# Kernel tuning notes

Hardware: AMD Instinct MI355X
Metric: run time of the kernel (lower is better)

## Reference

```python
import jax, jax.numpy as jnp
import numpy as np

N_NODES = 100000
N_EDGES = 1600000
IN_DIM = 128
HID = 128
N_CLS = 10
N_GRAPHS = 128


def setup_inputs() -> dict:
    key = jax.random.key(0)
    ks = jax.random.split(key, 8)
    x = jax.random.normal(ks[0], (N_NODES, IN_DIM), dtype=jnp.float32)
    edge_index = jax.random.randint(ks[1], (2, N_EDGES), 0, N_NODES, dtype=jnp.int64)
    batch = jnp.sort(jax.random.randint(ks[2], (N_NODES,), 0, N_GRAPHS, dtype=jnp.int64))
    # GCNConv weights (PyG uses glorot; scale approximated) and biases
    W1 = jax.random.normal(ks[3], (IN_DIM, HID), dtype=jnp.float32) * (1.0 / np.sqrt(IN_DIM))
    b1 = jnp.zeros((HID,), dtype=jnp.float32)
    W2 = jax.random.normal(ks[4], (HID, HID), dtype=jnp.float32) * (1.0 / np.sqrt(HID))
    b2 = jnp.zeros((HID,), dtype=jnp.float32)
    Wlin = jax.random.normal(ks[5], (HID, N_CLS), dtype=jnp.float32) * (1.0 / np.sqrt(HID))
    blin = jnp.zeros((N_CLS,), dtype=jnp.float32)
    return {"x": x, "edge_index": edge_index, "batch": batch,
            "W1": W1, "b1": b1, "W2": W2, "b2": b2, "Wlin": Wlin, "blin": blin}


def _gcn_norm(edge_index, n_nodes):
    # PyG GCNConv default: add self-loops, symmetric D^-1/2 A D^-1/2 normalization
    loop = jnp.arange(n_nodes, dtype=edge_index.dtype)
    row = jnp.concatenate([edge_index[0], loop])  # source nodes
    col = jnp.concatenate([edge_index[1], loop])  # destination nodes
    ones = jnp.ones(col.shape[0], dtype=jnp.float32)
    deg = jax.ops.segment_sum(ones, col, num_segments=n_nodes)
    dinv = jnp.where(deg > 0, jax.lax.rsqrt(deg), 0.0)
    norm = dinv[row] * dinv[col]  # per-edge normalization coefficient
    return row, col, norm


def _gcn_conv(x, W, b, row, col, norm, n_nodes):
    h = x @ W                                   # [N, hid] dense transform first (small hid)
    msg = h[row] * norm[:, None]                # gather + scale over edges
    out = jax.ops.segment_sum(msg, col, num_segments=n_nodes)  # scatter-add aggregation
    return out + b


def reference(x, edge_index, batch, W1, b1, W2, b2, Wlin, blin):
    n = x.shape[0]
    row, col, norm = _gcn_norm(edge_index, n)
    h = jax.nn.relu(_gcn_conv(x, W1, b1, row, col, norm, n))
    h = jax.nn.relu(_gcn_conv(h, W2, b2, row, col, norm, n))
    # global_mean_pool over batch ids
    sums = jax.ops.segment_sum(h, batch, num_segments=N_GRAPHS)
    cnts = jax.ops.segment_sum(jnp.ones((n,), dtype=h.dtype), batch, num_segments=N_GRAPHS)
    pooled = sums / jnp.maximum(cnts, 1.0)[:, None]
    return pooled @ Wlin + blin  # [N_GRAPHS, n_cls]
```

## Files before the change

### kernel.cpp

```cpp
#include <hip/hip_runtime.h>

#define NN 100000
#define NE 1600000
#define DD 128
#define NG 128
#define NC 10
#define AGG_WAVES 8192
#define POOL_WAVES 2048

#define B1SH 8
#define NB1 ((NN + 255) / 256)
#define EPB 8192
#define NWG1 ((NE + EPB - 1) / EPB)
#define GEMM_BLOCKS ((NN + 63) / 64)

typedef __attribute__((ext_vector_type(8))) short short8v;
typedef __attribute__((ext_vector_type(4))) float f32x4;

__device__ __forceinline__ unsigned short f2bf(float f) {
    unsigned int u = __float_as_uint(f);
    u = (u + 0x7fffu + ((u >> 16) & 1u)) >> 16;
    return (unsigned short)u;
}
__device__ __forceinline__ float bflo(unsigned int p) { return __uint_as_float(p << 16); }
__device__ __forceinline__ float bfhi(unsigned int p) { return __uint_as_float(p & 0xffff0000u); }

__global__ __launch_bounds__(256) void hist_k(const int* __restrict__ col, int* __restrict__ hist) {
    __shared__ int lh[NB1];
    int t = threadIdx.x, w = blockIdx.x;
    for (int i = t; i < NB1; i += 256) lh[i] = 0;
    __syncthreads();
    int base = w * EPB;
    int lim = min(base + EPB, NE);
#pragma unroll 4
    for (int e = base + t; e < lim; e += 256) atomicAdd(&lh[col[e] >> B1SH], 1);
    __syncthreads();
    for (int i = t; i < NB1; i += 256) hist[i * NWG1 + w] = lh[i];
}

__global__ __launch_bounds__(512) void btot_k(const int* __restrict__ hist, int* __restrict__ bbase) {
    __shared__ int tmp[512];
    int t = threadIdx.x;
    int s = 0;
    if (t < NB1) {
        const int* hp = hist + t * NWG1;
        for (int w = 0; w < NWG1; ++w) s += hp[w];
    }
    tmp[t] = s;
    __syncthreads();
    for (int o = 1; o < 512; o <<= 1) {
        int v = (t >= o) ? tmp[t - o] : 0;
        __syncthreads();
        tmp[t] += v;
        __syncthreads();
    }
    if (t < NB1) bbase[t] = tmp[t] - s;
    if (t == 511) bbase[NB1] = tmp[511];
}

__global__ __launch_bounds__(256) void histscan_k(const int* __restrict__ bbase, int* __restrict__ hist) {
    __shared__ int tmp[256];
    int b = blockIdx.x, t = threadIdx.x;
    int v = (t < NWG1) ? hist[b * NWG1 + t] : 0;
    tmp[t] = v;
    __syncthreads();
    for (int o = 1; o < 256; o <<= 1) {
        int u = (t >= o) ? tmp[t - o] : 0;
        __syncthreads();
        tmp[t] += u;
        __syncthreads();
    }
    int excl = tmp[t] - v;
    if (t < NWG1) hist[b * NWG1 + t] = bbase[b] + excl;
}

__global__ __launch_bounds__(256) void part1_k(const int* __restrict__ row, const int* __restrict__ col,
                                               const int* __restrict__ hist, int* __restrict__ tmpe) {
    __shared__ int lcur[NB1];
    int t = threadIdx.x, w = blockIdx.x;
    for (int i = t; i < NB1; i += 256) lcur[i] = hist[i * NWG1 + w];
    __syncthreads();
    int base = w * EPB;
    int lim = min(base + EPB, NE);
#pragma unroll 4
    for (int e = base + t; e < lim; e += 256) {
        int c = col[e];
        int pos = atomicAdd(&lcur[c >> B1SH], 1);
        tmpe[pos] = (row[e] << B1SH) | (c & 255);
    }
}

__global__ __launch_bounds__(512) void part2b_k(const int* __restrict__ bbase, const int* __restrict__ tmpe,
                                                unsigned int* __restrict__ csr_src, int* __restrict__ offs,
                                                float* __restrict__ dinv) {
    __shared__ int lcnt[256];
    __shared__ int lsc[256];
    int b = blockIdx.x, t = threadIdx.x;
    if (t < 256) lcnt[t] = 0;
    __syncthreads();
    int ebeg = bbase[b], eend = bbase[b + 1];
    for (int e = ebeg + t; e < eend; e += 512) atomicAdd(&lcnt[tmpe[e] & 255], 1);
    __syncthreads();
    if (t < 256) lsc[t] = lcnt[t];
    __syncthreads();
    for (int o = 1; o < 256; o <<= 1) {
        int v = (t < 256 && t >= o) ? lsc[t - o] : 0;
        __syncthreads();
        if (t < 256) lsc[t] += v;
        __syncthreads();
    }
    int n0 = b << B1SH;
    if (t < 256) {
        int node = n0 + t;
        if (node < NN) {
            int excl = lsc[t] - lcnt[t];
            offs[node] = ebeg + excl;
            dinv[node] = rsqrtf((float)lcnt[t] + 1.0f);
        }
    }
    if (b == NB1 - 1 && t == 0) offs[NN] = NE;
    __syncthreads();
    if (t < 256) lsc[t] = ebeg + (lsc[t] - lcnt[t]);
    __syncthreads();
    for (int e = ebeg + t; e < eend; e += 512) {
        int p = tmpe[e];
        int pos = atomicAdd(&lsc[p & 255], 1);
        csr_src[pos] = (unsigned int)(p >> B1SH) << 6;
    }
}

__global__ __launch_bounds__(256) void pack_w2_k(const float* __restrict__ W1, const float* __restrict__ W2,
                                                 unsigned short* __restrict__ Wpk1,
                                                 unsigned short* __restrict__ Wpk2,
                                                 float* __restrict__ gsum) {
    int t = threadIdx.x;
    if (blockIdx.x == 2) {
        float4* g4 = (float4*)gsum;
        for (int i = t; i < NG * DD / 4; i += 256) g4[i] = make_float4(0, 0, 0, 0);
        return;
    }
    const float* W = blockIdx.x ? W2 : W1;
    unsigned short* Wpk = blockIdx.x ? Wpk2 : Wpk1;
    for (int f = t * 64; f < t * 64 + 64; ++f) {
        int j = f & 7, lane = (f >> 3) & 63, kk = (f >> 9) & 3, n = f >> 11;
        int k = kk * 32 + ((lane >> 4) << 3) + j;
        int c = n * 16 + (lane & 15);
        Wpk[f] = f2bf(W[k * DD + c]);
    }
}

template <int IN_BF16>
__global__ __launch_bounds__(256) void gemm_mfma_k(const void* __restrict__ Xv,
                                                   const unsigned short* __restrict__ Wpk,
                                                   const float* __restrict__ dinv,
                                                   unsigned short* __restrict__ outb) {
    __shared__ unsigned short wlds[16384];
    int tid = threadIdx.x;
    const uint4* wg = (const uint4*)Wpk;
    uint4* wl = (uint4*)wlds;
#pragma unroll
    for (int i = 0; i < 8; ++i) wl[tid + i * 256] = wg[tid + i * 256];
    __syncthreads();

    int w = tid >> 6, lane = tid & 63;
    int kg = lane >> 4;
    int rowbase = blockIdx.x * 64 + w * 16;
    int rl = min(rowbase + (lane & 15), NN - 1);

    short8v a[4];
    if (IN_BF16) {
        const unsigned short* xb = (const unsigned short*)Xv;
#pragma unroll
        for (int kk = 0; kk < 4; ++kk)
            a[kk] = *(const short8v*)(xb + (long)rl * DD + kk * 32 + kg * 8);
    } else {
        const float* xf = (const float*)Xv;
#pragma unroll
        for (int kk = 0; kk < 4; ++kk) {
            float4 f0 = *(const float4*)(xf + (long)rl * DD + kk * 32 + kg * 8);
            float4 f1 = *(const float4*)(xf + (long)rl * DD + kk * 32 + kg * 8 + 4);
            short8v t;
            t[0] = (short)f2bf(f0.x); t[1] = (short)f2bf(f0.y);
            t[2] = (short)f2bf(f0.z); t[3] = (short)f2bf(f0.w);
            t[4] = (short)f2bf(f1.x); t[5] = (short)f2bf(f1.y);
            t[6] = (short)f2bf(f1.z); t[7] = (short)f2bf(f1.w);
            a[kk] = t;
        }
    }

    f32x4 acc[8];
#pragma unroll
    for (int n = 0; n < 8; ++n) acc[n] = (f32x4){0.f, 0.f, 0.f, 0.f};
#pragma unroll
    for (int n = 0; n < 8; ++n) {
#pragma unroll
        for (int kk = 0; kk < 4; ++kk) {
            short8v b = *(const short8v*)(wlds + ((n * 4 + kk) * 64 + lane) * 8);
            acc[n] = __builtin_amdgcn_mfma_f32_16x16x32_bf16(a[kk], b, acc[n], 0, 0, 0);
        }
    }

    int c0 = lane & 15;
#pragma unroll
    for (int reg = 0; reg < 4; ++reg) {
        int row = rowbase + kg * 4 + reg;
        if (row < NN) {
            float dv = dinv[row];
            unsigned short* op = outb + (long)row * DD + c0;
#pragma unroll
            for (int n = 0; n < 8; ++n) op[n * 16] = f2bf(dv * acc[n][reg]);
        }
    }
}

__global__ __launch_bounds__(256) void agg_k(const unsigned int* __restrict__ hpb,
                                             const float* __restrict__ dinv,
                                             const int* __restrict__ offs,
                                             const unsigned int* __restrict__ csr,
                                             const float* __restrict__ bias,
                                             unsigned short* __restrict__ outb) {
    int wv = (blockIdx.x << 2) + (threadIdx.x >> 6);
    unsigned int lane = threadIdx.x & 63;
    float2 bb = ((const float2*)bias)[lane];
    for (int node = wv; node < NN; node += AGG_WAVES) {
        int s = offs[node];
        int e_end = offs[node + 1];
        unsigned int ps = hpb[(unsigned int)node * 64u + lane];
        float accx = bflo(ps);
        float accy = bfhi(ps);
        int e = s;
        for (; e + 8 <= e_end; e += 8) {
            unsigned int p0 = hpb[csr[e] + lane];
            unsigned int p1 = hpb[csr[e + 1] + lane];
            unsigned int p2 = hpb[csr[e + 2] + lane];
            unsigned int p3 = hpb[csr[e + 3] + lane];
            unsigned int p4 = hpb[csr[e + 4] + lane];
            unsigned int p5 = hpb[csr[e + 5] + lane];
            unsigned int p6 = hpb[csr[e + 6] + lane];
            unsigned int p7 = hpb[csr[e + 7] + lane];
            accx += (bflo(p0) + bflo(p1)) + (bflo(p2) + bflo(p3)) +
                    (bflo(p4) + bflo(p5)) + (bflo(p6) + bflo(p7));
            accy += (bfhi(p0) + bfhi(p1)) + (bfhi(p2) + bfhi(p3)) +
                    (bfhi(p4) + bfhi(p5)) + (bfhi(p6) + bfhi(p7));
        }
        if (e + 4 <= e_end) {
            unsigned int p0 = hpb[csr[e] + lane];
            unsigned int p1 = hpb[csr[e + 1] + lane];
            unsigned int p2 = hpb[csr[e + 2] + lane];
            unsigned int p3 = hpb[csr[e + 3] + lane];
            accx += (bflo(p0) + bflo(p1)) + (bflo(p2) + bflo(p3));
            accy += (bfhi(p0) + bfhi(p1)) + (bfhi(p2) + bfhi(p3));
            e += 4;
        }
        for (; e < e_end; ++e) {
            unsigned int p0 = hpb[csr[e] + lane];
            accx += bflo(p0);
            accy += bfhi(p0);
        }
        float dv = dinv[node];
        float ox = fmaxf(fmaf(dv, accx, bb.x), 0.0f);
        float oy = fmaxf(fmaf(dv, accy, bb.y), 0.0f);
        ((ushort2*)outb)[(unsigned int)node * 64u + lane] = make_ushort2(f2bf(ox), f2bf(oy));
    }
}

__global__ __launch_bounds__(256) void pool2_k(const unsigned short* __restrict__ h,
                                               const int* __restrict__ batch,
                                               float* __restrict__ gsum) {
    int wave = (blockIdx.x * 256 + threadIdx.x) >> 6;
    int lane = threadIdx.x & 63;
    const int per = (NN + POOL_WAVES - 1) / POOL_WAVES;
    int s = wave * per;
    int e = min(s + per, NN);
    if (s >= e) return;
    const unsigned int* h2 = (const unsigned int*)h;
    float2 acc = {0.0f, 0.0f};
    int cur = batch[s];
    for (int r = s; r < e; ++r) {
        int b = batch[r];
        if (b != cur) {
            atomicAdd(&gsum[cur * DD + 2 * lane], acc.x);
            atomicAdd(&gsum[cur * DD + 2 * lane + 1], acc.y);
            acc.x = 0.0f; acc.y = 0.0f;
            cur = b;
        }
        unsigned int v = h2[(unsigned int)r * 64u + lane];
        acc.x += bflo(v);
        acc.y += bfhi(v);
    }
    atomicAdd(&gsum[cur * DD + 2 * lane], acc.x);
    atomicAdd(&gsum[cur * DD + 2 * lane + 1], acc.y);
}

__global__ __launch_bounds__(256) void final_k(const float* __restrict__ gsum, const int* __restrict__ batch,
                                               const float* __restrict__ Wlin, const float* __restrict__ blin,
                                               float* __restrict__ out) {
    int idx = blockIdx.x * 256 + threadIdx.x;
    if (idx >= NG * NC) return;
    int g = idx / NC, c = idx % NC;
    int s0, s1;
    {
        int lo = 0, hi = NN;
        while (lo < hi) { int m = (lo + hi) >> 1; if (batch[m] < g) lo = m + 1; else hi = m; }
        s0 = lo;
        lo = s0; hi = NN;
        while (lo < hi) { int m = (lo + hi) >> 1; if (batch[m] < g + 1) lo = m + 1; else hi = m; }
        s1 = lo;
    }
    int cnt = s1 - s0;
    float inv = 1.0f / fmaxf((float)cnt, 1.0f);
    float acc = blin[c];
    for (int k = 0; k < DD; ++k) acc = fmaf(gsum[g * DD + k] * inv, Wlin[k * NC + c], acc);
    out[idx] = acc;
}

extern "C" void kernel_launch(void* const* d_in, const int* in_sizes, int n_in,
                              void* d_out, int out_size, void* d_ws, size_t ws_size,
                              hipStream_t stream) {
    const float* x     = (const float*)d_in[0];
    const int*   ei    = (const int*)d_in[1];
    const int*   batch = (const int*)d_in[2];
    const float* W1    = (const float*)d_in[3];
    const float* b1    = (const float*)d_in[4];
    const float* W2    = (const float*)d_in[5];
    const float* b2    = (const float*)d_in[6];
    const float* Wlin  = (const float*)d_in[7];
    const float* blin  = (const float*)d_in[8];
    float* out = (float*)d_out;

    const int* erow = ei;
    const int* ecol = ei + NE;

    char* ws = (char*)d_ws;
    size_t off = 0;
    auto alloc = [&](size_t bytes) {
        void* p = ws + off;
        off = (off + bytes + 255) & ~(size_t)255;
        return p;
    };
    unsigned short* hbuf  = (unsigned short*)alloc((size_t)NN * DD * 2);
    unsigned short* habuf = (unsigned short*)alloc((size_t)NN * DD * 2);
    unsigned short* Wpk1  = (unsigned short*)alloc(16384 * 2);
    unsigned short* Wpk2  = (unsigned short*)alloc(16384 * 2);
    float* dinv     = (float*)alloc(NN * 4);
    int*   offs     = (int*)alloc((NN + 1) * 4);
    int*   bbase    = (int*)alloc((NB1 + 1) * 4);
    int*   hist     = (int*)alloc((size_t)NB1 * NWG1 * 4);
    int*   tmpe     = (int*)alloc((size_t)NE * 4);
    unsigned int* csrsrc = (unsigned int*)alloc((size_t)NE * 4);
    float* gsum     = (float*)alloc(NG * DD * 4);
    (void)ws_size; (void)in_sizes; (void)n_in; (void)out_size;

    pack_w2_k<<<3, 256, 0, stream>>>(W1, W2, Wpk1, Wpk2, gsum);
    hist_k<<<NWG1, 256, 0, stream>>>(ecol, hist);
    btot_k<<<1, 512, 0, stream>>>(hist, bbase);
    histscan_k<<<NB1, 256, 0, stream>>>(bbase, hist);
    part1_k<<<NWG1, 256, 0, stream>>>(erow, ecol, hist, tmpe);
    part2b_k<<<NB1, 512, 0, stream>>>(bbase, tmpe, csrsrc, offs, dinv);

    gemm_mfma_k<0><<<GEMM_BLOCKS, 256, 0, stream>>>(x, Wpk1, dinv, hbuf);
    agg_k<<<AGG_WAVES / 4, 256, 0, stream>>>((const unsigned int*)hbuf, dinv, offs, csrsrc, b1, habuf);
    gemm_mfma_k<1><<<GEMM_BLOCKS, 256, 0, stream>>>(habuf, Wpk2, dinv, hbuf);
    agg_k<<<AGG_WAVES / 4, 256, 0, stream>>>((const unsigned int*)hbuf, dinv, offs, csrsrc, b2, habuf);

    pool2_k<<<POOL_WAVES / 4, 256, 0, stream>>>(habuf, batch, gsum);
    final_k<<<(NG * NC + 255) / 256, 256, 0, stream>>>(gsum, batch, Wlin, blin, out);
}
```

Before: 265.7 us.

## Fuse first GEMM with edge histogram and second aggregation with mean pooling

The first layer's x@W1 GEMM now runs in the same launch as the edge histogram, as separate blocks, so it no longer waits for the CSR build. Because dinv is not ready at that point, a new scale kernel applies the dinv row scaling afterwards. The second aggregation now accumulates pooled sums directly instead of writing the full hidden tensor and reading it back in a separate pool kernel. Trade-offs: an extra read-modify-write pass over hbuf for scaling, a bf16 rounding of the unscaled GEMM output before scaling, and contiguous node ranges per wave in the fused aggregation, which may balance load worse than the strided assignment.

```diff
diff --git a/kernel.cpp b/kernel.cpp
--- a/kernel.cpp
+++ b/kernel.cpp
@@ -6,7 +6,6 @@
 #define NG 128
 #define NC 10
 #define AGG_WAVES 8192
-#define POOL_WAVES 2048
 
 #define B1SH 8
 #define NB1 ((NN + 255) / 256)
@@ -25,17 +24,145 @@
 __device__ __forceinline__ float bflo(unsigned int p) { return __uint_as_float(p << 16); }
 __device__ __forceinline__ float bfhi(unsigned int p) { return __uint_as_float(p & 0xffff0000u); }
 
-__global__ __launch_bounds__(256) void hist_k(const int* __restrict__ col, int* __restrict__ hist) {
-    __shared__ int lh[NB1];
-    int t = threadIdx.x, w = blockIdx.x;
-    for (int i = t; i < NB1; i += 256) lh[i] = 0;
-    __syncthreads();
-    int base = w * EPB;
-    int lim = min(base + EPB, NE);
+template <int IN_BF16>
+__device__ __forceinline__ void gemm_body(const void* __restrict__ Xv,
+                                          const unsigned short* __restrict__ Wpk,
+                                          const float* __restrict__ dinv,
+                                          unsigned short* __restrict__ outb, int blk,
+                                          unsigned short* wlds) {
+    int tid = threadIdx.x;
+    const uint4* wg = (const uint4*)Wpk;
+    uint4* wl = (uint4*)wlds;
+#pragma unroll
+    for (int i = 0; i < 8; ++i) wl[tid + i * 256] = wg[tid + i * 256];
+    __syncthreads();
+
+    int w = tid >> 6, lane = tid & 63;
+    int kg = lane >> 4;
+    int rowbase = blk * 64 + w * 16;
+    int rl = min(rowbase + (lane & 15), NN - 1);
+
+    short8v a[4];
+    if (IN_BF16) {
+        const unsigned short* xb = (const unsigned short*)Xv;
+#pragma unroll
+        for (int kk = 0; kk < 4; ++kk)
+            a[kk] = *(const short8v*)(xb + (long)rl * DD + kk * 32 + kg * 8);
+    } else {
+        const float* xf = (const float*)Xv;
+#pragma unroll
+        for (int kk = 0; kk < 4; ++kk) {
+            float4 f0 = *(const float4*)(xf + (long)rl * DD + kk * 32 + kg * 8);
+            float4 f1 = *(const float4*)(xf + (long)rl * DD + kk * 32 + kg * 8 + 4);
+            short8v t;
+            t[0] = (short)f2bf(f0.x); t[1] = (short)f2bf(f0.y);
+            t[2] = (short)f2bf(f0.z); t[3] = (short)f2bf(f0.w);
+            t[4] = (short)f2bf(f1.x); t[5] = (short)f2bf(f1.y);
+            t[6] = (short)f2bf(f1.z); t[7] = (short)f2bf(f1.w);
+            a[kk] = t;
+        }
+    }
+
+    f32x4 acc[8];
+#pragma unroll
+    for (int n = 0; n < 8; ++n) acc[n] = (f32x4){0.f, 0.f, 0.f, 0.f};
+#pragma unroll
+    for (int n = 0; n < 8; ++n) {
+#pragma unroll
+        for (int kk = 0; kk < 4; ++kk) {
+            short8v b = *(const short8v*)(wlds + ((n * 4 + kk) * 64 + lane) * 8);
+            acc[n] = __builtin_amdgcn_mfma_f32_16x16x32_bf16(a[kk], b, acc[n], 0, 0, 0);
+        }
+    }
+
+    int c0 = lane & 15;
+#pragma unroll
+    for (int reg = 0; reg < 4; ++reg) {
+        int row = rowbase + kg * 4 + reg;
+        if (row < NN) {
+            float dv = dinv[row];
+            unsigned short* op = outb + (long)row * DD + c0;
+#pragma unroll
+            for (int n = 0; n < 8; ++n) op[n * 16] = f2bf(dv * acc[n][reg]);
+        }
+    }
+}
+
+__global__ __launch_bounds__(256) void k1_fused(const int* __restrict__ col, int* __restrict__ hist,
+                                                const float* __restrict__ x,
+                                                const unsigned short* __restrict__ Wpk1,
+                                                unsigned short* __restrict__ hbuf) {
+    __shared__ unsigned short wlds[16384];
+    int bid = blockIdx.x, t = threadIdx.x;
+    if (bid < NWG1) {
+        int* lh = (int*)wlds;
+        for (int i = t; i < NB1; i += 256) lh[i] = 0;
+        __syncthreads();
+        int base = bid * EPB;
+        int lim = min(base + EPB, NE);
 #pragma unroll 4
-    for (int e = base + t; e < lim; e += 256) atomicAdd(&lh[col[e] >> B1SH], 1);
-    __syncthreads();
-    for (int i = t; i < NB1; i += 256) hist[i * NWG1 + w] = lh[i];
+        for (int e = base + t; e < lim; e += 256) atomicAdd(&lh[col[e] >> B1SH], 1);
+        __syncthreads();
+        for (int i = t; i < NB1; i += 256) hist[i * NWG1 + bid] = lh[i];
+    } else {
+        int tid = threadIdx.x;
+        const uint4* wg = (const uint4*)Wpk1;
+        uint4* wl = (uint4*)wlds;
+#pragma unroll
+        for (int i = 0; i < 8; ++i) wl[tid + i * 256] = wg[tid + i * 256];
+        __syncthreads();
+        int w = tid >> 6, lane = tid & 63;
+        int kg = lane >> 4;
+        int blk = bid - NWG1;
+        int rowbase = blk * 64 + w * 16;
+        int rl = min(rowbase + (lane & 15), NN - 1);
+        short8v a[4];
+        const float* xf = x;
+#pragma unroll
+        for (int kk = 0; kk < 4; ++kk) {
+            float4 f0 = *(const float4*)(xf + (long)rl * DD + kk * 32 + kg * 8);
+            float4 f1 = *(const float4*)(xf + (long)rl * DD + kk * 32 + kg * 8 + 4);
+            short8v tv;
+            tv[0] = (short)f2bf(f0.x); tv[1] = (short)f2bf(f0.y);
+            tv[2] = (short)f2bf(f0.z); tv[3] = (short)f2bf(f0.w);
+            tv[4] = (short)f2bf(f1.x); tv[5] = (short)f2bf(f1.y);
+            tv[6] = (short)f2bf(f1.z); tv[7] = (short)f2bf(f1.w);
+            a[kk] = tv;
+        }
+        f32x4 acc[8];
+#pragma unroll
+        for (int n = 0; n < 8; ++n) acc[n] = (f32x4){0.f, 0.f, 0.f, 0.f};
+#pragma unroll
+        for (int n = 0; n < 8; ++n) {
+#pragma unroll
+            for (int kk = 0; kk < 4; ++kk) {
+                short8v b = *(const short8v*)(wlds + ((n * 4 + kk) * 64 + lane) * 8);
+                acc[n] = __builtin_amdgcn_mfma_f32_16x16x32_bf16(a[kk], b, acc[n], 0, 0, 0);
+            }
+        }
+        int c0 = lane & 15;
+#pragma unroll
+        for (int reg = 0; reg < 4; ++reg) {
+            int row = rowbase + kg * 4 + reg;
+            if (row < NN) {
+                unsigned short* op = hbuf + (long)row * DD + c0;
+#pragma unroll
+                for (int n = 0; n < 8; ++n) op[n * 16] = f2bf(acc[n][reg]);
+            }
+        }
+    }
+}
+
+__global__ __launch_bounds__(256) void scale1_k(unsigned int* __restrict__ hpb,
+                                                const float* __restrict__ dinv) {
+    int wv = (blockIdx.x << 2) + (threadIdx.x >> 6);
+    unsigned int lane = threadIdx.x & 63;
+    for (int row = wv; row < NN; row += AGG_WAVES) {
+        float dv = dinv[row];
+        unsigned int p = hpb[(unsigned int)row * 64u + lane];
+        hpb[(unsigned int)row * 64u + lane] =
+            ((unsigned int)f2bf(dv * bflo(p))) | ((unsigned int)f2bf(dv * bfhi(p)) << 16);
+    }
 }
 
 __global__ __launch_bounds__(512) void btot_k(const int* __restrict__ hist, int* __restrict__ bbase) {
@@ -149,67 +276,46 @@
     }
 }
 
-template <int IN_BF16>
-__global__ __launch_bounds__(256) void gemm_mfma_k(const void* __restrict__ Xv,
-                                                   const unsigned short* __restrict__ Wpk,
-                                                   const float* __restrict__ dinv,
-                                                   unsigned short* __restrict__ outb) {
+__global__ __launch_bounds__(256) void gemm2_k(const unsigned short* __restrict__ xb,
+                                               const unsigned short* __restrict__ Wpk,
+                                               const float* __restrict__ dinv,
+                                               unsigned short* __restrict__ outb) {
     __shared__ unsigned short wlds[16384];
-    int tid = threadIdx.x;
-    const uint4* wg = (const uint4*)Wpk;
-    uint4* wl = (uint4*)wlds;
-#pragma unroll
-    for (int i = 0; i < 8; ++i) wl[tid + i * 256] = wg[tid + i * 256];
-    __syncthreads();
-
-    int w = tid >> 6, lane = tid & 63;
-    int kg = lane >> 4;
-    int rowbase = blockIdx.x * 64 + w * 16;
-    int rl = min(rowbase + (lane & 15), NN - 1);
-
-    short8v a[4];
-    if (IN_BF16) {
-        const unsigned short* xb = (const unsigned short*)Xv;
-#pragma unroll
-        for (int kk = 0; kk < 4; ++kk)
-            a[kk] = *(const short8v*)(xb + (long)rl * DD + kk * 32 + kg * 8);
-    } else {
-        const float* xf = (const float*)Xv;
-#pragma unroll
-        for (int kk = 0; kk < 4; ++kk) {
-            float4 f0 = *(const float4*)(xf + (long)rl * DD + kk * 32 + kg * 8);
-            float4 f1 = *(const float4*)(xf + (long)rl * DD + kk * 32 + kg * 8 + 4);
-            short8v t;
-            t[0] = (short)f2bf(f0.x); t[1] = (short)f2bf(f0.y);
-            t[2] = (short)f2bf(f0.z); t[3] = (short)f2bf(f0.w);
-            t[4] = (short)f2bf(f1.x); t[5] = (short)f2bf(f1.y);
-            t[6] = (short)f2bf(f1.z); t[7] = (short)f2bf(f1.w);
-            a[kk] = t;
-        }
-    }
-
-    f32x4 acc[8];
-#pragma unroll
-    for (int n = 0; n < 8; ++n) acc[n] = (f32x4){0.f, 0.f, 0.f, 0.f};
-#pragma unroll
-    for (int n = 0; n < 8; ++n) {
-#pragma unroll
-        for (int kk = 0; kk < 4; ++kk) {
-            short8v b = *(const short8v*)(wlds + ((n * 4 + kk) * 64 + lane) * 8);
-            acc[n] = __builtin_amdgcn_mfma_f32_16x16x32_bf16(a[kk], b, acc[n], 0, 0, 0);
-        }
-    }
-
-    int c0 = lane & 15;
-#pragma unroll
-    for (int reg = 0; reg < 4; ++reg) {
-        int row = rowbase + kg * 4 + reg;
-        if (row < NN) {
-            float dv = dinv[row];
-            unsigned short* op = outb + (long)row * DD + c0;
-#pragma unroll
-            for (int n = 0; n < 8; ++n) op[n * 16] = f2bf(dv * acc[n][reg]);
-        }
+    gemm_body<1>(xb, Wpk, dinv, outb, blockIdx.x, wlds);
+}
+
+__device__ __forceinline__ void agg_node(const unsigned int* __restrict__ hpb,
+                                         const unsigned int* __restrict__ csr,
+                                         int s, int e_end, unsigned int lane,
+                                         float& accx, float& accy) {
+    int e = s;
+    for (; e + 8 <= e_end; e += 8) {
+        unsigned int p0 = hpb[csr[e] + lane];
+        unsigned int p1 = hpb[csr[e + 1] + lane];
+        unsigned int p2 = hpb[csr[e + 2] + lane];
+        unsigned int p3 = hpb[csr[e + 3] + lane];
+        unsigned int p4 = hpb[csr[e + 4] + lane];
+        unsigned int p5 = hpb[csr[e + 5] + lane];
+        unsigned int p6 = hpb[csr[e + 6] + lane];
+        unsigned int p7 = hpb[csr[e + 7] + lane];
+        accx += (bflo(p0) + bflo(p1)) + (bflo(p2) + bflo(p3)) +
+                (bflo(p4) + bflo(p5)) + (bflo(p6) + bflo(p7));
+        accy += (bfhi(p0) + bfhi(p1)) + (bfhi(p2) + bfhi(p3)) +
+                (bfhi(p4) + bfhi(p5)) + (bfhi(p6) + bfhi(p7));
+    }
+    if (e + 4 <= e_end) {
+        unsigned int p0 = hpb[csr[e] + lane];
+        unsigned int p1 = hpb[csr[e + 1] + lane];
+        unsigned int p2 = hpb[csr[e + 2] + lane];
+        unsigned int p3 = hpb[csr[e + 3] + lane];
+        accx += (bflo(p0) + bflo(p1)) + (bflo(p2) + bflo(p3));
+        accy += (bfhi(p0) + bfhi(p1)) + (bfhi(p2) + bfhi(p3));
+        e += 4;
+    }
+    for (; e < e_end; ++e) {
+        unsigned int p0 = hpb[csr[e] + lane];
+        accx += bflo(p0);
+        accy += bfhi(p0);
     }
 }
 
@@ -223,40 +329,9 @@
     unsigned int lane = threadIdx.x & 63;
     float2 bb = ((const float2*)bias)[lane];
     for (int node = wv; node < NN; node += AGG_WAVES) {
-        int s = offs[node];
-        int e_end = offs[node + 1];
         unsigned int ps = hpb[(unsigned int)node * 64u + lane];
-        float accx = bflo(ps);
-        float accy = bfhi(ps);
-        int e = s;
-        for (; e + 8 <= e_end; e += 8) {
-            unsigned int p0 = hpb[csr[e] + lane];
-            unsigned int p1 = hpb[csr[e + 1] + lane];
-            unsigned int p2 = hpb[csr[e + 2] + lane];
-            unsigned int p3 = hpb[csr[e + 3] + lane];
-            unsigned int p4 = hpb[csr[e + 4] + lane];
-            unsigned int p5 = hpb[csr[e + 5] + lane];
-            unsigned int p6 = hpb[csr[e + 6] + lane];
-            unsigned int p7 = hpb[csr[e + 7] + lane];
-            accx += (bflo(p0) + bflo(p1)) + (bflo(p2) + bflo(p3)) +
-                    (bflo(p4) + bflo(p5)) + (bflo(p6) + bflo(p7));
-            accy += (bfhi(p0) + bfhi(p1)) + (bfhi(p2) + bfhi(p3)) +
-                    (bfhi(p4) + bfhi(p5)) + (bfhi(p6) + bfhi(p7));
-        }
-        if (e + 4 <= e_end) {
-            unsigned int p0 = hpb[csr[e] + lane];
-            unsigned int p1 = hpb[csr[e + 1] + lane];
-            unsigned int p2 = hpb[csr[e + 2] + lane];
-            unsigned int p3 = hpb[csr[e + 3] + lane];
-            accx += (bflo(p0) + bflo(p1)) + (bflo(p2) + bflo(p3));
-            accy += (bfhi(p0) + bfhi(p1)) + (bfhi(p2) + bfhi(p3));
-            e += 4;
-        }
-        for (; e < e_end; ++e) {
-            unsigned int p0 = hpb[csr[e] + lane];
-            accx += bflo(p0);
-            accy += bfhi(p0);
-        }
+        float accx = bflo(ps), accy = bfhi(ps);
+        agg_node(hpb, csr, offs[node], offs[node + 1], lane, accx, accy);
         float dv = dinv[node];
         float ox = fmaxf(fmaf(dv, accx, bb.x), 0.0f);
         float oy = fmaxf(fmaf(dv, accy, bb.y), 0.0f);
@@ -264,29 +339,36 @@
     }
 }
 
-__global__ __launch_bounds__(256) void pool2_k(const unsigned short* __restrict__ h,
-                                               const int* __restrict__ batch,
-                                               float* __restrict__ gsum) {
-    int wave = (blockIdx.x * 256 + threadIdx.x) >> 6;
-    int lane = threadIdx.x & 63;
-    const int per = (NN + POOL_WAVES - 1) / POOL_WAVES;
+__global__ __launch_bounds__(256) void agg2pool_k(const unsigned int* __restrict__ hpb,
+                                                  const float* __restrict__ dinv,
+                                                  const int* __restrict__ offs,
+                                                  const unsigned int* __restrict__ csr,
+                                                  const float* __restrict__ bias,
+                                                  const int* __restrict__ batch,
+                                                  float* __restrict__ gsum) {
+    int wave = (blockIdx.x << 2) + (threadIdx.x >> 6);
+    unsigned int lane = threadIdx.x & 63;
+    const int per = (NN + AGG_WAVES - 1) / AGG_WAVES;
     int s = wave * per;
     int e = min(s + per, NN);
     if (s >= e) return;
-    const unsigned int* h2 = (const unsigned int*)h;
+    float2 bb = ((const float2*)bias)[lane];
     float2 acc = {0.0f, 0.0f};
     int cur = batch[s];
-    for (int r = s; r < e; ++r) {
-        int b = batch[r];
-        if (b != cur) {
+    for (int node = s; node < e; ++node) {
+        int bg = batch[node];
+        if (bg != cur) {
             atomicAdd(&gsum[cur * DD + 2 * lane], acc.x);
             atomicAdd(&gsum[cur * DD + 2 * lane + 1], acc.y);
             acc.x = 0.0f; acc.y = 0.0f;
-            cur = b;
-        }
-        unsigned int v = h2[(unsigned int)r * 64u + lane];
-        acc.x += bflo(v);
-        acc.y += bfhi(v);
+            cur = bg;
+        }
+        unsigned int ps = hpb[(unsigned int)node * 64u + lane];
+        float accx = bflo(ps), accy = bfhi(ps);
+        agg_node(hpb, csr, offs[node], offs[node + 1], lane, accx, accy);
+        float dv = dinv[node];
+        acc.x += fmaxf(fmaf(dv, accx, bb.x), 0.0f);
+        acc.y += fmaxf(fmaf(dv, accy, bb.y), 0.0f);
     }
     atomicAdd(&gsum[cur * DD + 2 * lane], acc.x);
     atomicAdd(&gsum[cur * DD + 2 * lane + 1], acc.y);
@@ -352,17 +434,16 @@
     (void)ws_size; (void)in_sizes; (void)n_in; (void)out_size;
 
     pack_w2_k<<<3, 256, 0, stream>>>(W1, W2, Wpk1, Wpk2, gsum);
-    hist_k<<<NWG1, 256, 0, stream>>>(ecol, hist);
+    k1_fused<<<NWG1 + GEMM_BLOCKS, 256, 0, stream>>>(ecol, hist, x, Wpk1, hbuf);
     btot_k<<<1, 512, 0, stream>>>(hist, bbase);
     histscan_k<<<NB1, 256, 0, stream>>>(bbase, hist);
     part1_k<<<NWG1, 256, 0, stream>>>(erow, ecol, hist, tmpe);
     part2b_k<<<NB1, 512, 0, stream>>>(bbase, tmpe, csrsrc, offs, dinv);
-
-    gemm_mfma_k<0><<<GEMM_BLOCKS, 256, 0, stream>>>(x, Wpk1, dinv, hbuf);
+    scale1_k<<<AGG_WAVES / 4, 256, 0, stream>>>((unsigned int*)hbuf, dinv);
+
     agg_k<<<AGG_WAVES / 4, 256, 0, stream>>>((const unsigned int*)hbuf, dinv, offs, csrsrc, b1, habuf);
-    gemm_mfma_k<1><<<GEMM_BLOCKS, 256, 0, stream>>>(habuf, Wpk2, dinv, hbuf);
-    agg_k<<<AGG_WAVES / 4, 256, 0, stream>>>((const unsigned int*)hbuf, dinv, offs, csrsrc, b2, habuf);
-
-    pool2_k<<<POOL_WAVES / 4, 256, 0, stream>>>(habuf, batch, gsum);
+    gemm2_k<<<GEMM_BLOCKS, 256, 0, stream>>>(habuf, Wpk2, dinv, hbuf);
+    agg2pool_k<<<AGG_WAVES / 4, 256, 0, stream>>>((const unsigned int*)hbuf, dinv, offs, csrsrc, b2,
+                                                  batch, gsum);
     final_k<<<(NG * NC + 255) / 256, 256, 0, stream>>>(gsum, batch, Wlin, blin, out);
 }
```

Result: faster. 243.6 us (-8.3%).
